# Performance work log

Hardware: AMD Instinct MI355X
Metric: run time of the kernel (lower is better)

## Reference

```python
import jax, jax.numpy as jnp
import numpy as np

B, S, N_CATE, N_CONT = 32, 1024, 4, 4
HIDDEN, ATTN, VOCAB, EMB = 1024, 512, 1000, 128


def sinusoidal_pe(seq_len, d_model, base=10000.0):
    pos = jnp.arange(seq_len, dtype=jnp.float32)[:, None]            # [S,1]
    i = jnp.arange(d_model // 2, dtype=jnp.float32)[None, :]         # [1,D/2]
    ang = pos / jnp.power(base, 2.0 * i / d_model)                   # [S,D/2]
    pe = jnp.zeros((seq_len, d_model), dtype=jnp.float32)
    pe = pe.at[:, 0::2].set(jnp.sin(ang))
    pe = pe.at[:, 1::2].set(jnp.cos(ang))
    return pe


def setup_inputs() -> dict:
    key = jax.random.key(0)
    ks = jax.random.split(key, 20)
    s = 0.02
    inp = {
        "cate_x": jax.random.randint(ks[0], (B, S, N_CATE), 0, VOCAB, dtype=jnp.int64)
                  if jax.config.read("jax_enable_x64") else
                  jax.random.randint(ks[0], (B, S, N_CATE), 0, VOCAB, dtype=jnp.int32),
        "cont_x": jax.random.normal(ks[1], (B, S, N_CONT), dtype=jnp.float32),
        "mask": jnp.ones((B, S), dtype=bool),
        "targets": jax.random.uniform(ks[2], (B, S), dtype=jnp.float32),
        # EntireEmbedding params: 4 cate tables + cont linear + comb projection
        "E0": jax.random.normal(ks[3], (VOCAB, EMB), dtype=jnp.float32) * s,
        "E1": jax.random.normal(ks[4], (VOCAB, EMB), dtype=jnp.float32) * s,
        "E2": jax.random.normal(ks[5], (VOCAB, EMB), dtype=jnp.float32) * s,
        "E3": jax.random.normal(ks[6], (VOCAB, EMB), dtype=jnp.float32) * s,
        "Wc": jax.random.normal(ks[7], (N_CONT, N_CATE * EMB), dtype=jnp.float32) * s,
        "Wproj": jax.random.normal(ks[8], (2 * N_CATE * EMB, HIDDEN), dtype=jnp.float32) * s,
        # two-head attention linears (bias=False)
        "WQ1": jax.random.normal(ks[9], (HIDDEN, ATTN), dtype=jnp.float32) * s,
        "WK1": jax.random.normal(ks[10], (HIDDEN, ATTN), dtype=jnp.float32) * s,
        "WV1": jax.random.normal(ks[11], (HIDDEN, ATTN), dtype=jnp.float32) * s,
        "WQ2": jax.random.normal(ks[12], (HIDDEN, ATTN), dtype=jnp.float32) * s,
        "WK2": jax.random.normal(ks[13], (HIDDEN, ATTN), dtype=jnp.float32) * s,
        "WV2": jax.random.normal(ks[14], (HIDDEN, ATTN), dtype=jnp.float32) * s,
        "W0": jax.random.normal(ks[15], (2 * ATTN, HIDDEN), dtype=jnp.float32) * s,
        "Wf": jax.random.normal(ks[16], (HIDDEN, 1), dtype=jnp.float32) * s,
    }
    return inp


def _attend(x, WQ, WK, WV):
    Q = x @ WQ  # [B,S,A]
    K = x @ WK
    V = x @ WV
    scores = jnp.einsum("bqd,bkd->bqk", Q, K) / jnp.sqrt(jnp.float32(ATTN))
    # faithful to nn.Softmax(dim=1): normalize over the QUERY axis
    attn = jax.nn.softmax(scores, axis=1)
    return jnp.einsum("bqk,bkv->bqv", attn, V)


def reference(cate_x, cont_x, mask, targets, E0, E1, E2, E3, Wc, Wproj,
              WQ1, WK1, WV1, WQ2, WK2, WV2, W0, Wf):
    # EntireEmbedding: per-feature cate embeddings + cont projection -> comb proj
    cate_emb = jnp.concatenate(
        [E0[cate_x[..., 0]], E1[cate_x[..., 1]], E2[cate_x[..., 2]], E3[cate_x[..., 3]]],
        axis=-1)                                   # [B,S,512]
    cont_emb = cont_x @ Wc                          # [B,S,512]
    x = jnp.concatenate([cate_emb, cont_emb], axis=-1) @ Wproj  # [B,S,H]
    x = x + sinusoidal_pe(x.shape[1], HIDDEN)[None, :, :]
    z1 = _attend(x, WQ1, WK1, WV1)                  # [B,S,A]
    z2 = _attend(x, WQ2, WK2, WV2)                  # [B,S,A]
    z = jnp.concatenate([z1, z2], axis=-1) @ W0     # [B,S,H]
    out = jax.nn.sigmoid(z @ Wf)                    # FinalConnecting: Linear(H,1)+sigmoid
    return out.squeeze(-1)                          # [B,S]
```

## Files before the change

kernel.cpp:

```cpp
#include <hip/hip_runtime.h>
#include <hip/hip_bf16.h>
#include <math.h>

#define BB    32
#define SS    1024
#define HID   1024
#define AT    512
#define NVOC  1000
#define NT    (BB*SS)

typedef unsigned short u16;
typedef __attribute__((ext_vector_type(8))) short s16x8;
typedef __attribute__((ext_vector_type(4))) float f32x4;

__device__ __forceinline__ float bf2f(u16 u) {
    union { unsigned int i; float f; } x; x.i = ((unsigned int)u) << 16; return x.f;
}
__device__ __forceinline__ u16 f2bf(float f) {
    union { float f; unsigned int i; } u; u.f = f;
    unsigned int r = u.i + 0x7fffu + ((u.i >> 16) & 1u);
    return (u16)(r >> 16);
}
__device__ __forceinline__ float4 ld4(const float* p) { return *(const float4*)p; }
__device__ __forceinline__ float4 ld4bf(const u16* p) {
    ushort4 v = *(const ushort4*)p;
    return make_float4(bf2f(v.x), bf2f(v.y), bf2f(v.z), bf2f(v.w));
}
__device__ __forceinline__ void unpack8(uint4 v, float* x) {
    x[0] = bf2f((u16)(v.x & 0xffff)); x[1] = bf2f((u16)(v.x >> 16));
    x[2] = bf2f((u16)(v.y & 0xffff)); x[3] = bf2f((u16)(v.y >> 16));
    x[4] = bf2f((u16)(v.z & 0xffff)); x[5] = bf2f((u16)(v.z >> 16));
    x[6] = bf2f((u16)(v.w & 0xffff)); x[7] = bf2f((u16)(v.w >> 16));
}

__device__ __forceinline__ void gld16(const u16* g, u16* l) {
    __builtin_amdgcn_global_load_lds(
        (const __attribute__((address_space(1))) unsigned int*)g,
        (__attribute__((address_space(3))) unsigned int*)l,
        16, 0, 0);
}

struct Ptrs4f { const float* p[4]; };

__device__ __forceinline__ float blockReduceSum(float x) {
    #pragma unroll
    for (int off = 32; off > 0; off >>= 1) x += __shfl_down(x, off, 64);
    __shared__ float tmp[4];
    int lane = threadIdx.x & 63, wid = threadIdx.x >> 6;
    if (lane == 0) tmp[wid] = x;
    __syncthreads();
    if (threadIdx.x == 0) x = tmp[0] + tmp[1] + tmp[2] + tmp[3];
    return x;
}
__device__ __forceinline__ float waveReduceSum(float x) {
    #pragma unroll
    for (int off = 32; off > 0; off >>= 1) x += __shfl_down(x, off, 64);
    return x;
}

__global__ void k_s1(Ptrs4f E, const float* __restrict__ Wproj, Ptrs4f W,
                     const float* __restrict__ W0, const float* __restrict__ Wf,
                     u16* __restrict__ PE16, u16* __restrict__ E16o, u16* __restrict__ Wp16,
                     u16* __restrict__ Wt, float* __restrict__ W0f,
                     float* __restrict__ Wcp, float* __restrict__ CQ) {
    int blk = blockIdx.x, tid = threadIdx.x;
    if (blk < 2048) {
        int idx = blk*256 + tid;
        int s = idx >> 9, i = idx & 511;
        const float l2_10000 = 13.287712379549449f;
        float denom = exp2f((2.f * (float)i / 1024.f) * l2_10000);
        float ang = (float)s / denom;
        unsigned int pack = ((unsigned int)f2bf(__cosf(ang)) << 16) | f2bf(__sinf(ang));
        *(unsigned int*)(PE16 + (size_t)s*1024 + 2*i) = pack;
    } else if (blk < 4048) {
        int id2 = blk - 2048;
        int f = id2 / 500;
        int i = (id2 % 500)*256 + tid;
        E16o[(size_t)f*128000 + i] = f2bf(E.p[f][i]);
    } else if (blk < 6096) {
        int i = (blk - 4048)*256 + tid;
        Wp16[i] = f2bf(Wproj[i]);
    } else if (blk < 8144) {
        int tb = blk - 6096;
        int mat = tb >> 9, t2 = tb & 511;
        int cx = t2 & 15, ry = t2 >> 4;
        int r0 = ry*32, c0 = cx*32;
        const float* in = W.p[mat];
        u16* out = Wt + (size_t)mat*1024*512;
        __shared__ float tt[32][33];
        int tx = tid & 31, ty8 = tid >> 5;
        #pragma unroll
        for (int it = 0; it < 4; ++it)
            tt[ty8 + it*8][tx] = in[(size_t)(r0 + ty8 + it*8)*512 + c0 + tx];
        __syncthreads();
        #pragma unroll
        for (int it = 0; it < 4; ++it)
            out[(size_t)(c0 + ty8 + it*8)*1024 + r0 + tx] = f2bf(tt[tx][ty8 + it*8]);
    } else if (blk < 8400) {
        int wave = tid >> 6, lane = tid & 63;
        int row = (blk - 8144)*4 + wave;
        const float* rp = W0 + (size_t)row*1024;
        float a = 0.f;
        #pragma unroll
        for (int i = 0; i < 16; ++i) {
            int j = i*64 + lane;
            a += rp[j] * Wf[j];
        }
        a = waveReduceSum(a);
        if (lane == 0) W0f[row] = a;
    } else {
        int idx = (blk - 8400)*256 + tid;
        if (idx < 4096) Wcp[idx] = 0.f;
        else CQ[idx - 4096] = 0.f;
    }
}

__global__ void k_s2(const float* __restrict__ Wc, const float* __restrict__ Wproj,
                     Ptrs4f W, const float* __restrict__ WV1, const float* __restrict__ WV2,
                     const float* __restrict__ W0f, float* __restrict__ Wcp, float* __restrict__ v) {
    int blk = blockIdx.x, tid = threadIdx.x;
    if (blk < 64) {
        int c = blk >> 4, ic = (blk >> 2) & 3, jc = blk & 3;
        int i = ic*256 + tid;
        float a = 0.f;
        for (int j = jc*128; j < jc*128 + 128; ++j)
            a += Wc[c*512 + j] * Wproj[(size_t)(512 + j)*1024 + i];
        atomicAdd(&Wcp[c*1024 + i], a);
    } else {
        int b2 = blk - 64;
        int h = b2 >> 10, i = b2 & 1023;
        const float* WV = h ? WV2 : WV1;
        const float* wf = W0f + h*512;
        float a = 0.f;
        for (int aa = tid; aa < 512; aa += 256) a += WV[(size_t)i*512 + aa] * wf[aa];
        a = blockReduceSum(a);
        if (tid == 0) v[h*1024 + i] = a;
    }
}

__device__ __forceinline__ void cstore(float* p, float v) { *p = v; }
__device__ __forceinline__ void cstore(u16* p, float v)   { *p = f2bf(v); }

template<typename CT, bool CTRANS>
__device__ __forceinline__ void mfma_gemm(const u16* __restrict__ A, const u16* __restrict__ B,
                                          CT* __restrict__ C, int M, int N, int K, float alpha,
                                          int m0, int n0) {
    __shared__ u16 As[128*64];
    __shared__ u16 Bs[128*64];
    const int tid = threadIdx.x;
    const int wave = tid >> 6, lane = tid & 63;
    const int quad = lane >> 4, l16 = lane & 15;
    const int wm = (wave >> 1)*64, wn = (wave & 1)*64;
    const int srow = lane >> 3;
    const int scol = ((lane & 7) ^ srow) * 8;
    f32x4 acc[4][4] = {};

    for (int k0 = 0; k0 < K; k0 += 64) {
        #pragma unroll
        for (int p = 0; p < 4; ++p) {
            int rb = wave*32 + p*8;
            gld16(A + (size_t)(m0 + rb + srow)*K + k0 + scol, As + rb*64);
            gld16(B + (size_t)(n0 + rb + srow)*K + k0 + scol, Bs + rb*64);
        }
        __syncthreads();
        #pragma unroll
        for (int kk = 0; kk < 2; ++kk) {
            s16x8 af[4], bf[4];
            #pragma unroll
            for (int i = 0; i < 4; ++i) {
                int row = wm + i*16 + l16;
                af[i] = *(const s16x8*)(As + row*64 + (((kk*4 + quad) ^ (row & 7)) * 8));
            }
            #pragma unroll
            for (int j = 0; j < 4; ++j) {
                int row = wn + j*16 + l16;
                bf[j] = *(const s16x8*)(Bs + row*64 + (((kk*4 + quad) ^ (row & 7)) * 8));
            }
            #pragma unroll
            for (int i = 0; i < 4; ++i)
                #pragma unroll
                for (int j = 0; j < 4; ++j)
                    acc[i][j] = __builtin_amdgcn_mfma_f32_16x16x32_bf16(af[i], bf[j], acc[i][j], 0, 0, 0);
        }
        __syncthreads();
    }
    #pragma unroll
    for (int i = 0; i < 4; ++i) {
        #pragma unroll
        for (int r = 0; r < 4; ++r) {
            int gm = m0 + wm + i*16 + quad*4 + r;
            if (gm < M) {
                #pragma unroll
                for (int j = 0; j < 4; ++j) {
                    int gn = n0 + wn + j*16 + l16;
                    if (CTRANS) cstore(C + (size_t)gn*M + gm, acc[i][j][r] * alpha);
                    else        cstore(C + (size_t)gm*N + gn, acc[i][j][r] * alpha);
                }
            }
        }
    }
}

__global__ __launch_bounds__(256) void k_s3(const u16* __restrict__ Wp16, const u16* __restrict__ Wt,
                                            u16* __restrict__ PWT,
                                            const u16* __restrict__ PE16, u16* __restrict__ PEQ16,
                                            Ptrs4f W, const float* __restrict__ Wcp, float* __restrict__ CQ,
                                            const float* __restrict__ Wproj, const float* __restrict__ v,
                                            float* __restrict__ pv) {
    int blk = blockIdx.x, tid = threadIdx.x;
    if (blk < 64) {
        int x = blk & 3, z = blk >> 2;
        int f = z >> 2, w = z & 3;
        mfma_gemm<u16,true>(Wp16 + (size_t)f*128*1024, Wt + (size_t)w*512*1024,
                            PWT + (size_t)z*512*128, 128, 512, 1024, 1.f, 0, x*128);
    } else if (blk < 192) {
        int idx = blk - 64;
        int w = idx >> 5, r2 = idx & 31, y = r2 >> 2, x = r2 & 3;
        mfma_gemm<u16,false>(PE16, Wt + (size_t)w*512*1024, PEQ16 + (size_t)w*1024*512,
                             1024, 512, 1024, 1.f, y*128, x*128);
    } else if (blk < 448) {
        int r = blk - 192;
        int ns = r & 1, wc = (r >> 1) & 15, jc = r >> 5;
        int w = wc & 3, c = wc >> 2; int n = ns*256 + tid;
        const float* Ww = W.p[w];
        float a = 0.f;
        for (int j = jc*128; j < jc*128 + 128; ++j) a += Wcp[c*1024 + j] * Ww[(size_t)j*512 + n];
        atomicAdd(&CQ[(size_t)(w*4 + c)*512 + n], a);
    } else {
        int b2 = blk - 448;
        int i = b2 & 127, fh = b2 >> 7; int f = fh >> 1, h = fh & 1;
        const float* row = Wproj + (size_t)(f*128 + i)*1024;
        const float* vh = v + h*1024;
        float a = 0.f;
        for (int j = tid; j < 1024; j += 256) a += row[j] * vh[j];
        a = blockReduceSum(a);
        if (tid == 0) pv[(size_t)fh*128 + i] = a;
    }
}

__global__ __launch_bounds__(256) void k_s4(const u16* __restrict__ E16, const u16* __restrict__ PWT,
                                            const u16* __restrict__ PE16,
                                            u16* __restrict__ TQK16,
                                            const float* __restrict__ Wcp, const float* __restrict__ v,
                                            const float* __restrict__ pv,
                                            float* __restrict__ Ut, float* __restrict__ pu, float* __restrict__ cu) {
    int blk = blockIdx.x, tid = threadIdx.x;
    int wave = tid >> 6, lane = tid & 63;
    if (blk < 512) {
        int z = blk >> 5, r = blk & 31, y = r >> 2, x = r & 3;
        int f = z >> 2;
        mfma_gemm<u16,false>(E16 + (size_t)f*128000, PWT + (size_t)z*512*128,
                   TQK16 + (size_t)z*1000*512, 1000, 512, 128, 1.f, y*128, x*128);
        return;
    }
    int id = blk - 512;
    if (id < 32) {
        int d = id*256 + tid;
        if (d < 8000) {
            int f = d / 2000, h = (d / 1000) & 1, r = d % 1000;
            const u16* er = E16 + ((size_t)f*1000 + r)*128;
            const float* pvp = pv + (size_t)(f*2 + h)*128;
            float a = 0.f;
            #pragma unroll
            for (int q = 0; q < 16; ++q) {
                float xv[8];
                unpack8(*(const uint4*)(er + q*8), xv);
                #pragma unroll
                for (int e = 0; e < 8; ++e) a += xv[e] * pvp[q*8 + e];
            }
            Ut[(size_t)(f*2 + h)*1000 + r] = a;
        }
    } else if (id < 544) {
        int d = (id - 32)*4 + wave;
        int h = d >> 10, s = d & 1023;
        float a = 0.f;
        #pragma unroll
        for (int half = 0; half < 2; ++half) {
            int k = half*512 + lane*8;
            float xv[8];
            unpack8(*(const uint4*)(PE16 + (size_t)s*1024 + k), xv);
            float4 b0 = ld4(v + h*1024 + k), b1 = ld4(v + h*1024 + k + 4);
            a += xv[0]*b0.x + xv[1]*b0.y + xv[2]*b0.z + xv[3]*b0.w
               + xv[4]*b1.x + xv[5]*b1.y + xv[6]*b1.z + xv[7]*b1.w;
        }
        a = waveReduceSum(a);
        if (lane == 0) pu[h*1024 + s] = a;
    } else {
        #pragma unroll
        for (int rep = 0; rep < 2; ++rep) {
            int d = wave*2 + rep;
            int h = d >> 2, c = d & 3;
            float a = 0.f;
            #pragma unroll
            for (int i = 0; i < 16; ++i) {
                int j = i*64 + lane;
                a += Wcp[c*1024 + j] * v[h*1024 + j];
            }
            a = waveReduceSum(a);
            if (lane == 0) cu[h*4 + c] = a;
        }
    }
}

__global__ __launch_bounds__(512, 2) void k_g_S256(
        const u16* __restrict__ Q, const u16* __restrict__ K,
        u16* __restrict__ Sb, float alpha,
        float* __restrict__ Pm, float* __restrict__ Pd, int b0) {
    __shared__ u16 As[2][16384];
    __shared__ u16 Bs[2][16384];
    const int tid = threadIdx.x;
    const int wave = tid >> 6, lane = tid & 63;
    const int quad = lane >> 4, l16 = lane & 15;
    const int wm = wave >> 2, wn = wave & 3;

    const int nwg = (int)gridDim.x;
    int fblk = (int)blockIdx.x;
    int qq = nwg >> 3, rr = nwg & 7;
    int xcd = fblk & 7, idx = fblk >> 3;
    int swz = (xcd < rr ? xcd*(qq + 1) : rr*(qq + 1) + (xcd - rr)*qq) + idx;
    int b = swz >> 4, tile = swz & 15;
    int m0 = (tile >> 2) << 8, n0 = (tile & 3) << 8;

    const u16* __restrict__ Ab = Q + (size_t)b*SS*AT;
    const u16* __restrict__ Bb = K + (size_t)b*SS*AT;
    u16* __restrict__ C = Sb + (size_t)b*SS*SS;

    const int srow = lane >> 3;
    const int scol = ((lane & 7) ^ srow) * 8;

    f32x4 acc[8][4] = {};

    auto stageA = [&](int kt, int q) {
        gld16(Ab + (size_t)(m0 + q*64 + wave*8 + srow)*AT + kt*64 + scol,
              &As[kt & 1][q*4096 + wave*512]);
    };
    auto stageB = [&](int kt, int q) {
        gld16(Bb + (size_t)(n0 + q*64 + wave*8 + srow)*AT + kt*64 + scol,
              &Bs[kt & 1][q*4096 + wave*512]);
    };

    s16x8 af[4][2];
    s16x8 bf[4][2];

    auto readA = [&](int c, int ih) {
        #pragma unroll
        for (int i2 = 0; i2 < 4; ++i2) {
            int row = wm*128 + (ih*4 + i2)*16 + l16;
            #pragma unroll
            for (int kk = 0; kk < 2; ++kk)
                af[i2][kk] = *(const s16x8*)(&As[c][row*64 + (((kk*4 + quad) ^ (row & 7)) * 8)]);
        }
    };
    auto readB2 = [&](int c, int jh) {
        #pragma unroll
        for (int j2 = 0; j2 < 2; ++j2) {
            int j = jh*2 + j2;
            int row = wn*64 + j*16 + l16;
            #pragma unroll
            for (int kk = 0; kk < 2; ++kk)
                bf[j][kk] = *(const s16x8*)(&Bs[c][row*64 + (((kk*4 + quad) ^ (row & 7)) * 8)]);
        }
    };
    auto mma16 = [&](int ih, int jh) {
        __builtin_amdgcn_s_setprio(1);
        #pragma unroll
        for (int i2 = 0; i2 < 4; ++i2)
            #pragma unroll
            for (int j2 = 0; j2 < 2; ++j2) {
                int i = ih*4 + i2, j = jh*2 + j2;
                acc[i][j] = __builtin_amdgcn_mfma_f32_16x16x32_bf16(af[i2][0], bf[j][0], acc[i][j], 0, 0, 0);
                acc[i][j] = __builtin_amdgcn_mfma_f32_16x16x32_bf16(af[i2][1], bf[j][1], acc[i][j], 0, 0, 0);
            }
        __builtin_amdgcn_s_setprio(0);
    };
    auto midsync = [&]() {
        __builtin_amdgcn_s_barrier();
        asm volatile("s_waitcnt lgkmcnt(0)" ::: "memory");
        __builtin_amdgcn_sched_barrier(0);
    };

    #pragma unroll
    for (int q = 0; q < 4; ++q) stageA(0, q);
    #pragma unroll
    for (int q = 0; q < 4; ++q) stageB(0, q);
    stageA(1, 0); stageA(1, 2);
    stageB(1, 0); stageB(1, 1); stageB(1, 2); stageB(1, 3);
    asm volatile("s_waitcnt vmcnt(6)" ::: "memory");
    __builtin_amdgcn_s_barrier();

    #pragma unroll
    for (int t = 0; t < 8; ++t) {
        const int c = t & 1;
        readA(c, 0);
        readB2(c, 0);
        if (t <= 6) { stageA(t + 1, 1); stageA(t + 1, 3); }
        midsync();
        mma16(0, 0);
        __builtin_amdgcn_s_barrier();
        readB2(c, 1);
        if (t <= 5) { stageA(t + 2, 0); stageA(t + 2, 2); }
        midsync();
        mma16(0, 1);
        __builtin_amdgcn_s_barrier();
        readA(c, 1);
        if (t <= 5) { stageB(t + 2, 0); stageB(t + 2, 1); }
        midsync();
        mma16(1, 0);
        __builtin_amdgcn_s_barrier();
        if (t <= 5) { stageB(t + 2, 2); stageB(t + 2, 3); }
        midsync();
        mma16(1, 1);
        if (t <= 5)      asm volatile("s_waitcnt vmcnt(6)" ::: "memory");
        else if (t == 6) asm volatile("s_waitcnt vmcnt(0)" ::: "memory");
        __builtin_amdgcn_sched_barrier(0);
        __builtin_amdgcn_s_barrier();
    }

    #pragma unroll
    for (int i = 0; i < 8; ++i) {
        #pragma unroll
        for (int r = 0; r < 4; ++r) {
            int gm = m0 + wm*128 + i*16 + quad*4 + r;
            u16 q0 = f2bf(acc[i][0][r] * alpha);
            u16 q1 = f2bf(acc[i][1][r] * alpha);
            u16 q2 = f2bf(acc[i][2][r] * alpha);
            u16 q3 = f2bf(acc[i][3][r] * alpha);
            acc[i][0][r] = bf2f(q0); acc[i][1][r] = bf2f(q1);
            acc[i][2][r] = bf2f(q2); acc[i][3][r] = bf2f(q3);
            unsigned int lo = (unsigned int)q0 | ((unsigned int)q1 << 16);
            unsigned int hi = (unsigned int)q2 | ((unsigned int)q3 << 16);
            *(uint2*)(C + (size_t)gm*SS + n0 + wn*64 + l16*4) = make_uint2(lo, hi);
        }
    }
    float* sM = (float*)&As[0][0];
    float* sS = (float*)&Bs[0][0];
    #pragma unroll
    for (int j = 0; j < 4; ++j) {
        float mx = -3.4e38f;
        #pragma unroll
        for (int i = 0; i < 8; ++i)
            #pragma unroll
            for (int r = 0; r < 4; ++r) mx = fmaxf(mx, acc[i][j][r]);
        mx = fmaxf(mx, __shfl_xor(mx, 16, 64));
        mx = fmaxf(mx, __shfl_xor(mx, 32, 64));
        float sm = 0.f;
        #pragma unroll
        for (int i = 0; i < 8; ++i)
            #pragma unroll
            for (int r = 0; r < 4; ++r) sm += exp2f(acc[i][j][r] - mx);
        sm += __shfl_xor(sm, 16, 64);
        sm += __shfl_xor(sm, 32, 64);
        if (quad == 0) { sM[wave*64 + j*16 + l16] = mx; sS[wave*64 + j*16 + l16] = sm; }
    }
    __syncthreads();
    if (tid < 256) {
        int c = tid, wq = c >> 6, cc = c & 63;
        float ma = sM[wq*64 + cc],       sa = sS[wq*64 + cc];
        float mb = sM[(4 + wq)*64 + cc], sb2 = sS[(4 + wq)*64 + cc];
        float mm = fmaxf(ma, mb);
        float ss = sa * exp2f(ma - mm) + sb2 * exp2f(mb - mm);
        size_t po = ((size_t)(b0 + b)*4 + (m0 >> 8))*1024;
        Pm[po + n0 + c] = mm;
        Pd[po + n0 + c] = ss;
    }
}

__global__ __launch_bounds__(256) void k_gather(
                         const int* __restrict__ cate, const float* __restrict__ cont,
                         const u16* __restrict__ TQK, const float* __restrict__ CQ,
                         const u16* __restrict__ PEQ, const float* __restrict__ Ut,
                         const float* __restrict__ cu, const float* __restrict__ pu,
                         u16* __restrict__ Qh, u16* __restrict__ Kh,
                         float* __restrict__ u, int h) {
    int tid = threadIdx.x;
    int g = blockIdx.x & 7;
    size_t t = (size_t)(blockIdx.x >> 3)*32 + (tid >> 3);
    int cslot = tid & 7;
    int s = (int)(t & 1023);
    int4 cc = *(const int4*)(cate + t*4);
    float4 cv = ld4(cont + t*4);
    int n = g*64 + cslot*8;
    #pragma unroll
    for (int e = 0; e < 2; ++e) {
        int w = 2*h + e;
        const u16* t0 = TQK + ((size_t)(0*4  + w)*1000 + cc.x)*512 + n;
        const u16* t1 = TQK + ((size_t)(1*4  + w)*1000 + cc.y)*512 + n;
        const u16* t2 = TQK + ((size_t)(2*4  + w)*1000 + cc.z)*512 + n;
        const u16* t3 = TQK + ((size_t)(3*4  + w)*1000 + cc.w)*512 + n;
        const u16* pq = PEQ + ((size_t)w*1024 + s)*512 + n;
        const float* cq = CQ + (size_t)w*2048 + n;
        float a0[8], a1[8], a2[8], a3[8], ap[8];
        unpack8(*(const uint4*)t0, a0); unpack8(*(const uint4*)t1, a1);
        unpack8(*(const uint4*)t2, a2); unpack8(*(const uint4*)t3, a3);
        unpack8(*(const uint4*)pq, ap);
        unsigned int pack[4];
        #pragma unroll
        for (int jp = 0; jp < 4; ++jp) {
            float x0, x1;
            #pragma unroll
            for (int half = 0; half < 2; ++half) {
                int j = jp*2 + half;
                float x = a0[j] + a1[j] + a2[j] + a3[j] + ap[j]
                        + cv.x*cq[j] + cv.y*cq[512+j] + cv.z*cq[1024+j] + cv.w*cq[1536+j];
                if (half == 0) x0 = x; else x1 = x;
            }
            pack[jp] = ((unsigned int)f2bf(x1) << 16) | f2bf(x0);
        }
        u16* op = (e ? Kh : Qh) + t*512 + n;
        *(uint4*)op = make_uint4(pack[0], pack[1], pack[2], pack[3]);
    }
    if (g == 0 && (tid & 7) == 0) {
        float uu = pu[h*1024 + s]
                 + Ut[(0*2 + h)*1000 + cc.x] + Ut[(1*2 + h)*1000 + cc.y]
                 + Ut[(2*2 + h)*1000 + cc.z] + Ut[(3*2 + h)*1000 + cc.w]
                 + cv.x*cu[h*4+0] + cv.y*cu[h*4+1] + cv.z*cu[h*4+2] + cv.w*cu[h*4+3];
        u[(size_t)h*NT + t] = uu;
    }
}

__global__ __launch_bounds__(1024) void k_logit(const u16* __restrict__ Sb,
                        const float* __restrict__ Pm, const float* __restrict__ Pd,
                        const float* __restrict__ u,
                        float* __restrict__ logits, float* __restrict__ out,
                        int b0, int mode) {
    __shared__ float wsm[8][128];
    int wave = threadIdx.x >> 6, lane = threadIdx.x & 63;
    size_t bi = (size_t)(gridDim.x - 1 - blockIdx.x);
    size_t tl0 = bi*16;
    size_t tabs0 = (size_t)b0*1024 + tl0;
    int ab = (int)(tabs0 >> 10);
    {
        int k = threadIdx.x;
        float mx = -3.4e38f;
        #pragma unroll
        for (int mt = 0; mt < 4; ++mt) mx = fmaxf(mx, Pm[((size_t)ab*4 + mt)*1024 + k]);
        float dd = 0.f;
        #pragma unroll
        for (int mt = 0; mt < 4; ++mt) dd += Pd[((size_t)ab*4 + mt)*1024 + k]
                                           * exp2f(Pm[((size_t)ab*4 + mt)*1024 + k] - mx);
        int q = (k & ~63) | (((k & 15) << 2) | ((k & 63) >> 4));
        wsm[q & 7][q >> 3] = u[(size_t)ab*1024 + k] / dd * exp2f(-mx);
    }
    __syncthreads();
    size_t tl = tl0 + wave;
    size_t tabs = tabs0 + wave;
    const u16* row = Sb + tl*1024;
    float acc = 0.f;
    #pragma unroll
    for (int half = 0; half < 2; ++half) {
        int k = lane*8 + half*512;
        int li = lane + half*64;
        float sv[8];
        unpack8(*(const uint4*)(row + k), sv);
        acc += exp2f(sv[0])*wsm[0][li] + exp2f(sv[1])*wsm[1][li]
             + exp2f(sv[2])*wsm[2][li] + exp2f(sv[3])*wsm[3][li]
             + exp2f(sv[4])*wsm[4][li] + exp2f(sv[5])*wsm[5][li]
             + exp2f(sv[6])*wsm[6][li] + exp2f(sv[7])*wsm[7][li];
    }
    acc = waveReduceSum(acc);
    if (lane == 0) {
        if (mode == 0) logits[tabs] = acc;
        else {
            float x = logits[tabs] + acc;
            out[tabs] = 1.f / (1.f + expf(-x));
        }
    }
}

extern "C" void kernel_launch(void* const* d_in, const int* in_sizes, int n_in,
                              void* d_out, int out_size, void* d_ws, size_t ws_size,
                              hipStream_t stream) {
    const int*   cate = (const int*)d_in[0];
    const float* cont = (const float*)d_in[1];
    Ptrs4f E; E.p[0] = (const float*)d_in[4]; E.p[1] = (const float*)d_in[5];
              E.p[2] = (const float*)d_in[6]; E.p[3] = (const float*)d_in[7];
    const float* Wc    = (const float*)d_in[8];
    const float* Wproj = (const float*)d_in[9];
    Ptrs4f W; W.p[0] = (const float*)d_in[10];
              W.p[1] = (const float*)d_in[11];
              W.p[2] = (const float*)d_in[13];
              W.p[3] = (const float*)d_in[14];
    const float* WV1 = (const float*)d_in[12];
    const float* WV2 = (const float*)d_in[15];
    const float* W0  = (const float*)d_in[16];
    const float* Wf  = (const float*)d_in[17];

    char* base = (char*)d_ws;
    size_t off = 0;
    auto alloc = [&](size_t bytes) { void* p = base + off; off += (bytes + 255) & ~(size_t)255; return p; };
    u16*   PE16  = (u16*)  alloc(1048576ull*2);
    u16*   E16   = (u16*)  alloc(4ull*1000*128*2);
    u16*   Wt    = (u16*)  alloc(4ull*512*1024*2);
    u16*   Wp16  = (u16*)  alloc(512ull*1024*2);
    u16*   PWT   = (u16*)  alloc(16ull*512*128*2);
    u16*   TQK16 = (u16*)  alloc(16ull*1000*512*2);
    u16*   PEQ16 = (u16*)  alloc(4ull*1024*512*2);
    float* Wcp   = (float*)alloc(4*1024*4);
    float* W0f   = (float*)alloc(1024*4);
    float* vv    = (float*)alloc(2*1024*4);
    float* CQ    = (float*)alloc(16*512*4);
    float* pvb   = (float*)alloc(8*128*4);
    float* Ut    = (float*)alloc(8*1000*4);
    float* cu    = (float*)alloc(8*4);
    float* pu    = (float*)alloc(2*1024*4);
    float* ubuf  = (float*)alloc(2ull*NT*4);
    u16*   Qh    = (u16*)  alloc((size_t)NT*512*2);
    u16*   Kh    = (u16*)  alloc((size_t)NT*512*2);
    float* Pm    = (float*)alloc(32ull*8*1024*4);
    float* Pd    = (float*)alloc(32ull*8*1024*4);
    float* logits= (float*)alloc((size_t)NT*4);
    size_t sChunkBytes = (size_t)SS*SS*2;
    size_t remain = (ws_size > off) ? (ws_size - off) : 0;
    int NB = (int)(remain / sChunkBytes);
    if (NB > 32) NB = 32;
    if (NB < 1) NB = 1;
    u16* Sbuf = (u16*)(base + off);

    const float alpha = 0.06375954951107036f;

    k_s1<<<8448, 256, 0, stream>>>(E, Wproj, W, W0, Wf, PE16, E16, Wp16, Wt, W0f, Wcp, CQ);
    k_s2<<<2112, 256, 0, stream>>>(Wc, Wproj, W, WV1, WV2, W0f, Wcp, vv);
    k_s3<<<1472, 256, 0, stream>>>(Wp16, Wt, PWT, PE16, PEQ16, W, Wcp, CQ, Wproj, vv, pvb);
    k_s4<<<1057, 256, 0, stream>>>(E16, PWT, PE16, TQK16, Wcp, vv, pvb, Ut, pu, cu);

    for (int h = 0; h < 2; ++h) {
        k_gather<<<8192, 256, 0, stream>>>(cate, cont, TQK16, CQ, PEQ16, Ut, cu, pu, Qh, Kh, ubuf, h);
        for (int b0 = 0; b0 < 32; b0 += NB) {
            int nb = (32 - b0 < NB) ? (32 - b0) : NB;
            k_g_S256<<<16*nb, 512, 0, stream>>>(Qh + (size_t)b0*SS*AT, Kh + (size_t)b0*SS*AT,
                                                Sbuf, alpha, Pm, Pd, b0);
            k_logit<<<nb*64, 1024, 0, stream>>>(Sbuf, Pm, Pd, ubuf + (size_t)h*NT,
                                                logits, (float*)d_out, b0, h);
        }
    }
}
```

Measured before the change: 337.8 us.

## Fuse head-0 logit pass with head-1 gather in one launch

When the score buffer holds all 32 batches, the head-0 logit reduction and the head-1 Q/K gather now run in a single kernel launch, split by block index. The two phases touch disjoint buffers, so they can overlap on the GPU and one launch boundary disappears. The CQ coefficient reads in the gather are also changed to vectorised float4 loads instead of scalar ones. In exchange the gather half now runs with 1024-thread blocks, which may change its occupancy. The code also carries two parallel paths, depending on workspace size.

```diff
diff --git a/kernel.cpp b/kernel.cpp
--- a/kernel.cpp
+++ b/kernel.cpp
@@ -465,17 +465,13 @@
     }
 }
 
-__global__ __launch_bounds__(256) void k_gather(
-                         const int* __restrict__ cate, const float* __restrict__ cont,
-                         const u16* __restrict__ TQK, const float* __restrict__ CQ,
-                         const u16* __restrict__ PEQ, const float* __restrict__ Ut,
-                         const float* __restrict__ cu, const float* __restrict__ pu,
-                         u16* __restrict__ Qh, u16* __restrict__ Kh,
-                         float* __restrict__ u, int h) {
-    int tid = threadIdx.x;
-    int g = blockIdx.x & 7;
-    size_t t = (size_t)(blockIdx.x >> 3)*32 + (tid >> 3);
-    int cslot = tid & 7;
+__device__ __forceinline__ void gather_body(
+        const int* __restrict__ cate, const float* __restrict__ cont,
+        const u16* __restrict__ TQK, const float* __restrict__ CQ,
+        const u16* __restrict__ PEQ, const float* __restrict__ Ut,
+        const float* __restrict__ cu, const float* __restrict__ pu,
+        u16* __restrict__ Qh, u16* __restrict__ Kh, float* __restrict__ u,
+        int h, size_t t, int cslot, int g, bool writeU) {
     int s = (int)(t & 1023);
     int4 cc = *(const int4*)(cate + t*4);
     float4 cv = ld4(cont + t*4);
@@ -493,6 +489,11 @@
         unpack8(*(const uint4*)t0, a0); unpack8(*(const uint4*)t1, a1);
         unpack8(*(const uint4*)t2, a2); unpack8(*(const uint4*)t3, a3);
         unpack8(*(const uint4*)pq, ap);
+        float q0[8], q1[8], q2[8], q3[8];
+        *(float4*)&q0[0] = ld4(cq);        *(float4*)&q0[4] = ld4(cq + 4);
+        *(float4*)&q1[0] = ld4(cq + 512);  *(float4*)&q1[4] = ld4(cq + 516);
+        *(float4*)&q2[0] = ld4(cq + 1024); *(float4*)&q2[4] = ld4(cq + 1028);
+        *(float4*)&q3[0] = ld4(cq + 1536); *(float4*)&q3[4] = ld4(cq + 1540);
         unsigned int pack[4];
         #pragma unroll
         for (int jp = 0; jp < 4; ++jp) {
@@ -501,7 +502,7 @@
             for (int half = 0; half < 2; ++half) {
                 int j = jp*2 + half;
                 float x = a0[j] + a1[j] + a2[j] + a3[j] + ap[j]
-                        + cv.x*cq[j] + cv.y*cq[512+j] + cv.z*cq[1024+j] + cv.w*cq[1536+j];
+                        + cv.x*q0[j] + cv.y*q1[j] + cv.z*q2[j] + cv.w*q3[j];
                 if (half == 0) x0 = x; else x1 = x;
             }
             pack[jp] = ((unsigned int)f2bf(x1) << 16) | f2bf(x0);
@@ -509,7 +510,7 @@
         u16* op = (e ? Kh : Qh) + t*512 + n;
         *(uint4*)op = make_uint4(pack[0], pack[1], pack[2], pack[3]);
     }
-    if (g == 0 && (tid & 7) == 0) {
+    if (writeU) {
         float uu = pu[h*1024 + s]
                  + Ut[(0*2 + h)*1000 + cc.x] + Ut[(1*2 + h)*1000 + cc.y]
                  + Ut[(2*2 + h)*1000 + cc.z] + Ut[(3*2 + h)*1000 + cc.w]
@@ -518,14 +519,15 @@
     }
 }
 
-__global__ __launch_bounds__(1024) void k_logit(const u16* __restrict__ Sb,
-                        const float* __restrict__ Pm, const float* __restrict__ Pd,
-                        const float* __restrict__ u,
-                        float* __restrict__ logits, float* __restrict__ out,
-                        int b0, int mode) {
-    __shared__ float wsm[8][128];
+__device__ __forceinline__ void logit_body(
+        const u16* __restrict__ Sb,
+        const float* __restrict__ Pm, const float* __restrict__ Pd,
+        const float* __restrict__ u,
+        float* __restrict__ logits, float* __restrict__ out,
+        int b0, int mode, int blk, int nblk, float* wsmBase) {
+    float (*wsm)[128] = (float (*)[128])wsmBase;
     int wave = threadIdx.x >> 6, lane = threadIdx.x & 63;
-    size_t bi = (size_t)(gridDim.x - 1 - blockIdx.x);
+    size_t bi = (size_t)(nblk - 1 - blk);
     size_t tl0 = bi*16;
     size_t tabs0 = (size_t)b0*1024 + tl0;
     int ab = (int)(tabs0 >> 10);
@@ -564,6 +566,54 @@
             float x = logits[tabs] + acc;
             out[tabs] = 1.f / (1.f + expf(-x));
         }
+    }
+}
+
+__global__ __launch_bounds__(256) void k_gather(
+                         const int* __restrict__ cate, const float* __restrict__ cont,
+                         const u16* __restrict__ TQK, const float* __restrict__ CQ,
+                         const u16* __restrict__ PEQ, const float* __restrict__ Ut,
+                         const float* __restrict__ cu, const float* __restrict__ pu,
+                         u16* __restrict__ Qh, u16* __restrict__ Kh,
+                         float* __restrict__ u, int h) {
+    int tid = threadIdx.x;
+    int g = blockIdx.x & 7;
+    size_t t = (size_t)(blockIdx.x >> 3)*32 + (tid >> 3);
+    gather_body(cate, cont, TQK, CQ, PEQ, Ut, cu, pu, Qh, Kh, u, h,
+                t, tid & 7, g, g == 0 && (tid & 7) == 0);
+}
+
+__global__ __launch_bounds__(1024) void k_logit(const u16* __restrict__ Sb,
+                        const float* __restrict__ Pm, const float* __restrict__ Pd,
+                        const float* __restrict__ u,
+                        float* __restrict__ logits, float* __restrict__ out,
+                        int b0, int mode) {
+    __shared__ float wsm[8][128];
+    logit_body(Sb, Pm, Pd, u, logits, out, b0, mode, (int)blockIdx.x, (int)gridDim.x,
+               &wsm[0][0]);
+}
+
+__global__ __launch_bounds__(1024) void k_logit_gather(
+        const u16* __restrict__ Sb,
+        const float* __restrict__ Pm, const float* __restrict__ Pd,
+        const float* __restrict__ ubuf,
+        float* __restrict__ logits, float* __restrict__ out,
+        const int* __restrict__ cate, const float* __restrict__ cont,
+        const u16* __restrict__ TQK, const float* __restrict__ CQ,
+        const u16* __restrict__ PEQ, const float* __restrict__ Ut,
+        const float* __restrict__ cu, const float* __restrict__ pu,
+        u16* __restrict__ Qh, u16* __restrict__ Kh, float* __restrict__ ub) {
+    __shared__ float wsm[8][128];
+    int blk = (int)blockIdx.x;
+    if (blk < 2048) {
+        logit_body(Sb, Pm, Pd, ubuf, logits, out, 0, 0, blk, 2048, &wsm[0][0]);
+    } else {
+        int gb = blk - 2048;
+        int tid = threadIdx.x;
+        int g = gb & 7;
+        size_t t = (size_t)(gb >> 3)*128 + (tid >> 3);
+        gather_body(cate, cont, TQK, CQ, PEQ, Ut, cu, pu, Qh, Kh, ub, 1,
+                    t, tid & 7, g, g == 0 && (tid & 7) == 0);
     }
 }
 
@@ -623,14 +673,24 @@
     k_s3<<<1472, 256, 0, stream>>>(Wp16, Wt, PWT, PE16, PEQ16, W, Wcp, CQ, Wproj, vv, pvb);
     k_s4<<<1057, 256, 0, stream>>>(E16, PWT, PE16, TQK16, Wcp, vv, pvb, Ut, pu, cu);
 
-    for (int h = 0; h < 2; ++h) {
-        k_gather<<<8192, 256, 0, stream>>>(cate, cont, TQK16, CQ, PEQ16, Ut, cu, pu, Qh, Kh, ubuf, h);
-        for (int b0 = 0; b0 < 32; b0 += NB) {
-            int nb = (32 - b0 < NB) ? (32 - b0) : NB;
-            k_g_S256<<<16*nb, 512, 0, stream>>>(Qh + (size_t)b0*SS*AT, Kh + (size_t)b0*SS*AT,
-                                                Sbuf, alpha, Pm, Pd, b0);
-            k_logit<<<nb*64, 1024, 0, stream>>>(Sbuf, Pm, Pd, ubuf + (size_t)h*NT,
-                                                logits, (float*)d_out, b0, h);
-        }
-    }
-}
+    if (NB == 32) {
+        k_gather<<<8192, 256, 0, stream>>>(cate, cont, TQK16, CQ, PEQ16, Ut, cu, pu, Qh, Kh, ubuf, 0);
+        k_g_S256<<<512, 512, 0, stream>>>(Qh, Kh, Sbuf, alpha, Pm, Pd, 0);
+        k_logit_gather<<<4096, 1024, 0, stream>>>(Sbuf, Pm, Pd, ubuf, logits, (float*)d_out,
+                                                  cate, cont, TQK16, CQ, PEQ16, Ut, cu, pu,
+                                                  Qh, Kh, ubuf);
+        k_g_S256<<<512, 512, 0, stream>>>(Qh, Kh, Sbuf, alpha, Pm, Pd, 0);
+        k_logit<<<2048, 1024, 0, stream>>>(Sbuf, Pm, Pd, ubuf + NT, logits, (float*)d_out, 0, 1);
+    } else {
+        for (int h = 0; h < 2; ++h) {
+            k_gather<<<8192, 256, 0, stream>>>(cate, cont, TQK16, CQ, PEQ16, Ut, cu, pu, Qh, Kh, ubuf, h);
+            for (int b0 = 0; b0 < 32; b0 += NB) {
+                int nb = (32 - b0 < NB) ? (32 - b0) : NB;
+                k_g_S256<<<16*nb, 512, 0, stream>>>(Qh + (size_t)b0*SS*AT, Kh + (size_t)b0*SS*AT,
+                                                    Sbuf, alpha, Pm, Pd, b0);
+                k_logit<<<nb*64, 1024, 0, stream>>>(Sbuf, Pm, Pd, ubuf + (size_t)h*NT,
+                                                    logits, (float*)d_out, b0, h);
+            }
+        }
+    }
+}
```

Result: no change. 341.0 us (median of 2 runs) (+1.0%).
